# Kernel tuning notes

Hardware: AMD Instinct MI355X
Metric: run time of the kernel (lower is better)

The kernel has to match this reference:

```python
import jax, jax.numpy as jnp
import numpy as np

WIN = 9
EPS = 1e-05


def _box_sum(x, win=WIN):
    # Separable 3D box-filter sum: mathematically identical to conv3d with a
    pad = win // 2
    for axis in range(3):  # spatial axes D, H, W
        kshape = [1, 1, 1]
        kshape[axis] = win
        filt = jnp.ones((1, 1, *kshape), dtype=x.dtype)  # OIDHW
        padding = [(pad, pad) if i == axis else (0, 0) for i in range(3)]
        x = jax.lax.conv_general_dilated(
            x, filt, window_strides=(1, 1, 1), padding=padding,
            dimension_numbers=('NCDHW', 'OIDHW', 'NCDHW'))
    return x


def setup_inputs() -> dict:
    key = jax.random.key(0)
    k1, k2 = jax.random.split(key)
    shape = (2, 1, 160, 192, 224)
    y_true = jax.random.uniform(k1, shape, dtype=jnp.float32)
    y_pred = jax.random.uniform(k2, shape, dtype=jnp.float32)
    return {"y_true": y_true, "y_pred": y_pred}


def reference(y_true, y_pred):
    ii, ji = y_true, y_pred
    win_size = jnp.asarray(float(WIN ** 3), dtype=ii.dtype)

    i_sum = _box_sum(ii)
    j_sum = _box_sum(ji)
    i2_sum = _box_sum(ii * ii)
    j2_sum = _box_sum(ji * ji)
    ij_sum = _box_sum(ii * ji)

    ui = i_sum / win_size
    uj = j_sum / win_size
    cross = ij_sum - uj * i_sum - ui * j_sum + ui * uj * win_size
    i_var = jnp.maximum(i2_sum - 2 * ui * i_sum + ui * ui * win_size, EPS)
    j_var = jnp.maximum(j2_sum - 2 * uj * j_sum + uj * uj * win_size, EPS)
    return -jnp.mean(cross * cross / (i_var * j_var))
```

## Files before the change

kernel.cpp:

```cpp
#include <hip/hip_runtime.h>

namespace {

constexpr int BD = 2;
constexpr int DD = 160, HH = 192, WW = 224;
constexpr float INV_WIN = 1.0f / 729.0f;
constexpr float EPSV = 1e-5f;

constexpr int TH = 16, TW = 16;
constexpr int DC = 16;
constexpr int NREAL = DC + 8;
constexpr int NSS = NREAL / 2;
constexpr int NCH = DD / DC;
constexpr int GX = WW / TW;
constexpr int GY = HH / TH;
constexpr int GZ = BD * NCH;
constexpr int NBLK = GX * GY * GZ;
constexpr double NTOT = (double)BD * DD * HH * WW;

constexpr int SR_FS = 452;
constexpr int SR_PL = 2280;
constexpr int SC_FS = 324;
constexpr int SC_PL = 1620;

}

__global__ __launch_bounds__(256)
void ncc_fused(const float* __restrict__ x, const float* __restrict__ y,
               float* __restrict__ bsum) {
  const int tid = threadIdx.x;
  const int w0 = blockIdx.x * TW;
  const int h0 = blockIdx.y * TH;
  const int zb = blockIdx.z;
  const int b  = zb / NCH;
  const int d0 = (zb - b * NCH) * DC;

  __shared__ __align__(16) float srowF[2 * SR_PL];
  __shared__ __align__(16) float scolF[2 * SC_PL];
  __shared__ float swsum[4];

  const bool s2a = tid < 192;
  const int p2  = tid / 96;
  const int t96 = tid - 96 * p2;
  const int r2  = t96 >> 2;
  const int seg = tid & 3;
  const int gh  = h0 - 4 + r2;
  const int gw0 = w0 - 4 + seg * 4;
  const bool hok = (unsigned)gh < (unsigned)HH;
  const bool fastw = (gw0 >= 0) && (gw0 + 11 < WW);
  const unsigned plane = (unsigned)HH * WW;

  auto prefetch = [&](int s, float4* vx, float4* vy) {
    const int din = d0 - 4 + s;
    const float4 z = make_float4(0.f, 0.f, 0.f, 0.f);
    vx[0] = vx[1] = vx[2] = z;
    vy[0] = vy[1] = vy[2] = z;
    if (s2a && hok && (s < NREAL) && (din >= 0) && (din < DD)) {
      const unsigned rb = ((unsigned)b * DD + (unsigned)din) * plane + (unsigned)gh * WW;
      if (fastw) {
        const float4* px = (const float4*)(x + rb + gw0);
        const float4* py = (const float4*)(y + rb + gw0);
        vx[0] = px[0]; vx[1] = px[1]; vx[2] = px[2];
        vy[0] = py[0]; vy[1] = py[1]; vy[2] = py[2];
      } else {
        float* fx = (float*)vx;
        float* fy = (float*)vy;
#pragma unroll
        for (int e = 0; e < 12; ++e) {
          const int gw = gw0 + e;
          if ((unsigned)gw < (unsigned)WW) {
            fx[e] = x[rb + gw];
            fy[e] = y[rb + gw];
          }
        }
      }
    }
  };

  const int ow = tid & 15;
  const int oh = tid >> 4;

  float rg0[9], rg1[9], rg2[9], rg3[9], rg4[9];
#pragma unroll
  for (int k = 0; k < 9; ++k) { rg0[k]=0.f; rg1[k]=0.f; rg2[k]=0.f; rg3[k]=0.f; rg4[k]=0.f; }
  float a0=0.f, a1=0.f, a2=0.f, a3=0.f, a4=0.f;
  float lsum = 0.0f;

  float4 px4[3], py4[3];
  prefetch(p2, px4, py4);

#pragma unroll
  for (int ss = 0; ss < NSS; ++ss) {
    const int sA = 2 * ss;
    const int sB = sA + 1;
    const int slA = sA % 9;
    const int slB = sB % 9;

    float4 nx4[3], ny4[3];
    prefetch(2 * (ss + 1) + p2, nx4, ny4);

    if (s2a) {
      float xv[12], yv[12];
#pragma unroll
      for (int k = 0; k < 3; ++k) {
        *(float4*)&xv[4 * k] = px4[k];
        *(float4*)&yv[4 * k] = py4[k];
      }
      float s0=0.f, s1=0.f, s2=0.f, s3=0.f, s4=0.f;
#pragma unroll
      for (int k = 0; k < 9; ++k) {
        s0 += xv[k]; s1 += yv[k];
        s2 = fmaf(xv[k], xv[k], s2);
        s3 = fmaf(yv[k], yv[k], s3);
        s4 = fmaf(xv[k], yv[k], s4);
      }
      float* wb = &srowF[p2 * SR_PL + (seg * 4) * 28 + r2];
      wb[0 * SR_FS] = s0; wb[1 * SR_FS] = s1; wb[2 * SR_FS] = s2;
      wb[3 * SR_FS] = s3; wb[4 * SR_FS] = s4;
#pragma unroll
      for (int t = 1; t < 4; ++t) {
        const float xn = xv[8 + t], xo = xv[t - 1];
        const float yn = yv[8 + t], yo = yv[t - 1];
        s0 += xn - xo;
        s1 += yn - yo;
        s2 += fmaf(xn, xn, -(xo * xo));
        s3 += fmaf(yn, yn, -(yo * yo));
        s4 += fmaf(xn, yn, -(xo * yo));
        float* wt = wb + t * 28;
        wt[0 * SR_FS] = s0; wt[1 * SR_FS] = s1; wt[2 * SR_FS] = s2;
        wt[3 * SR_FS] = s3; wt[4 * SR_FS] = s4;
      }
    }
    __syncthreads();

    if (tid < 160) {
      const int p3  = tid / 80;
      const int r3  = tid - 80 * p3;
      const int f3  = r3 >> 4;
      const int wl3 = r3 & 15;
      const float* rp = &srowF[p3 * SR_PL + f3 * SR_FS + wl3 * 28];
      float rv[24];
#pragma unroll
      for (int t = 0; t < 6; ++t) *(float4*)&rv[4 * t] = *(const float4*)&rp[4 * t];
      float acc = rv[0];
#pragma unroll
      for (int t = 1; t < 9; ++t) acc += rv[t];
      float ov[16];
      ov[0] = acc;
#pragma unroll
      for (int o = 1; o < 16; ++o) { acc += rv[o + 8] - rv[o - 1]; ov[o] = acc; }
      float* cp = &scolF[p3 * SC_PL + f3 * SC_FS + wl3 * 20];
#pragma unroll
      for (int t = 0; t < 4; ++t)
        *(float4*)&cp[4 * t] = make_float4(ov[4*t], ov[4*t+1], ov[4*t+2], ov[4*t+3]);
    }
    __syncthreads();

    const float* cA = &scolF[ow * 20 + oh];
    const float* cB = cA + SC_PL;
    const float gA0 = cA[0*SC_FS], gA1 = cA[1*SC_FS], gA2 = cA[2*SC_FS],
                gA3 = cA[3*SC_FS], gA4 = cA[4*SC_FS];
    const float gB0 = cB[0*SC_FS], gB1 = cB[1*SC_FS], gB2 = cB[2*SC_FS],
                gB3 = cB[3*SC_FS], gB4 = cB[4*SC_FS];

    a0 += gA0 - rg0[slA]; rg0[slA] = gA0;
    a1 += gA1 - rg1[slA]; rg1[slA] = gA1;
    a2 += gA2 - rg2[slA]; rg2[slA] = gA2;
    a3 += gA3 - rg3[slA]; rg3[slA] = gA3;
    a4 += gA4 - rg4[slA]; rg4[slA] = gA4;
    if (sA >= 8) {
      const float cross = fmaf(-a0 * INV_WIN, a1, a4);
      const float iv = fmaxf(fmaf(-a0 * INV_WIN, a0, a2), EPSV);
      const float jv = fmaxf(fmaf(-a1 * INV_WIN, a1, a3), EPSV);
      lsum += (cross * cross) / (iv * jv);
    }
    a0 += gB0 - rg0[slB]; rg0[slB] = gB0;
    a1 += gB1 - rg1[slB]; rg1[slB] = gB1;
    a2 += gB2 - rg2[slB]; rg2[slB] = gB2;
    a3 += gB3 - rg3[slB]; rg3[slB] = gB3;
    a4 += gB4 - rg4[slB]; rg4[slB] = gB4;
    if (sB >= 8) {
      const float cross = fmaf(-a0 * INV_WIN, a1, a4);
      const float iv = fmaxf(fmaf(-a0 * INV_WIN, a0, a2), EPSV);
      const float jv = fmaxf(fmaf(-a1 * INV_WIN, a1, a3), EPSV);
      lsum += (cross * cross) / (iv * jv);
    }

#pragma unroll
    for (int k = 0; k < 3; ++k) { px4[k] = nx4[k]; py4[k] = ny4[k]; }
  }

#pragma unroll
  for (int off = 32; off > 0; off >>= 1) lsum += __shfl_down(lsum, off);
  if ((tid & 63) == 0) swsum[tid >> 6] = lsum;
  __syncthreads();
  if (tid == 0) {
    const int bid = ((int)blockIdx.z * GY + (int)blockIdx.y) * GX + (int)blockIdx.x;
    bsum[bid] = swsum[0] + swsum[1] + swsum[2] + swsum[3];
  }
}

__global__ __launch_bounds__(256)
void ncc_finalize(const float* __restrict__ bsum, float* __restrict__ out) {
  double s = 0.0;
  for (int i = threadIdx.x; i < NBLK; i += 256) s += (double)bsum[i];
#pragma unroll
  for (int off = 32; off > 0; off >>= 1) s += __shfl_down(s, off);
  __shared__ double sh[4];
  if ((threadIdx.x & 63) == 0) sh[threadIdx.x >> 6] = s;
  __syncthreads();
  if (threadIdx.x == 0)
    out[0] = (float)(-(sh[0] + sh[1] + sh[2] + sh[3]) / NTOT);
}

extern "C" void kernel_launch(void* const* d_in, const int* in_sizes, int n_in,
                              void* d_out, int out_size, void* d_ws, size_t ws_size,
                              hipStream_t stream) {
  const float* x = (const float*)d_in[0];
  const float* y = (const float*)d_in[1];
  float* bsum = (float*)d_ws;
  float* out  = (float*)d_out;

  dim3 grid(GX, GY, GZ);
  ncc_fused<<<grid, dim3(256), 0, stream>>>(x, y, bsum);
  ncc_finalize<<<1, dim3(256), 0, stream>>>(bsum, out);
}
```

Measured before the change: 211.1 us.

## Software-pipeline row, column and depth stages with one barrier per slice

The old loop handled two depth slices per iteration with two barriers, and all threads waited between the row-sum, column-sum and depth-accumulate stages. The new loop processes one slice per step and staggers the three stages across slices. Warps 0-1 do row sums for slice s, warps 2-3 do column sums for slice s-1, and all threads accumulate depth for slice s-2, with double-buffered shared memory and a single barrier per step. This lets the stages run concurrently on different warps, at the cost of 26 steps instead of 12 and fewer threads doing row sums per step.

```diff
diff --git a/kernel.cpp b/kernel.cpp
--- a/kernel.cpp
+++ b/kernel.cpp
@@ -10,7 +10,7 @@
 constexpr int TH = 16, TW = 16;
 constexpr int DC = 16;
 constexpr int NREAL = DC + 8;
-constexpr int NSS = NREAL / 2;
+constexpr int NSTEP = NREAL + 2;
 constexpr int NCH = DD / DC;
 constexpr int GX = WW / TW;
 constexpr int GY = HH / TH;
@@ -19,9 +19,9 @@
 constexpr double NTOT = (double)BD * DD * HH * WW;
 
 constexpr int SR_FS = 452;
-constexpr int SR_PL = 2280;
+constexpr int SR_BUF = 2280;
 constexpr int SC_FS = 324;
-constexpr int SC_PL = 1620;
+constexpr int SC_BUF = 1620;
 
 }
 
@@ -35,14 +35,12 @@
   const int b  = zb / NCH;
   const int d0 = (zb - b * NCH) * DC;
 
-  __shared__ __align__(16) float srowF[2 * SR_PL];
-  __shared__ __align__(16) float scolF[2 * SC_PL];
+  __shared__ __align__(16) float srowF[2][SR_BUF];
+  __shared__ __align__(16) float scolF[2][SC_BUF];
   __shared__ float swsum[4];
 
-  const bool s2a = tid < 192;
-  const int p2  = tid / 96;
-  const int t96 = tid - 96 * p2;
-  const int r2  = t96 >> 2;
+  const bool s2a = tid < 96;
+  const int r2  = tid >> 2;
   const int seg = tid & 3;
   const int gh  = h0 - 4 + r2;
   const int gw0 = w0 - 4 + seg * 4;
@@ -77,6 +75,11 @@
     }
   };
 
+  const bool s3a = (tid >= 128) && (tid < 208);
+  const int t3  = tid - 128;
+  const int f3  = t3 >> 4;
+  const int wl3 = t3 & 15;
+
   const int ow = tid & 15;
   const int oh = tid >> 4;
 
@@ -87,19 +90,33 @@
   float lsum = 0.0f;
 
   float4 px4[3], py4[3];
-  prefetch(p2, px4, py4);
-
-#pragma unroll
-  for (int ss = 0; ss < NSS; ++ss) {
-    const int sA = 2 * ss;
-    const int sB = sA + 1;
-    const int slA = sA % 9;
-    const int slB = sB % 9;
-
+  prefetch(0, px4, py4);
+
+#pragma unroll
+  for (int s = 0; s < NSTEP; ++s) {
     float4 nx4[3], ny4[3];
-    prefetch(2 * (ss + 1) + p2, nx4, ny4);
-
-    if (s2a) {
+    prefetch(s + 1, nx4, ny4);
+
+    if (s >= 2) {
+      const int ps = s - 2;
+      const int sl = ps % 9;
+      const float* cp = &scolF[ps & 1][ow * 20 + oh];
+      const float g0 = cp[0*SC_FS], g1 = cp[1*SC_FS], g2 = cp[2*SC_FS],
+                  g3 = cp[3*SC_FS], g4 = cp[4*SC_FS];
+      a0 += g0 - rg0[sl]; rg0[sl] = g0;
+      a1 += g1 - rg1[sl]; rg1[sl] = g1;
+      a2 += g2 - rg2[sl]; rg2[sl] = g2;
+      a3 += g3 - rg3[sl]; rg3[sl] = g3;
+      a4 += g4 - rg4[sl]; rg4[sl] = g4;
+      if (ps >= 8) {
+        const float cross = fmaf(-a0 * INV_WIN, a1, a4);
+        const float iv = fmaxf(fmaf(-a0 * INV_WIN, a0, a2), EPSV);
+        const float jv = fmaxf(fmaf(-a1 * INV_WIN, a1, a3), EPSV);
+        lsum += (cross * cross) / (iv * jv);
+      }
+    }
+
+    if (s < NREAL && s2a) {
       float xv[12], yv[12];
 #pragma unroll
       for (int k = 0; k < 3; ++k) {
@@ -114,7 +131,7 @@
         s3 = fmaf(yv[k], yv[k], s3);
         s4 = fmaf(xv[k], yv[k], s4);
       }
-      float* wb = &srowF[p2 * SR_PL + (seg * 4) * 28 + r2];
+      float* wb = &srowF[s & 1][(seg * 4) * 28 + r2];
       wb[0 * SR_FS] = s0; wb[1 * SR_FS] = s1; wb[2 * SR_FS] = s2;
       wb[3 * SR_FS] = s3; wb[4 * SR_FS] = s4;
 #pragma unroll
@@ -131,14 +148,9 @@
         wt[3 * SR_FS] = s3; wt[4 * SR_FS] = s4;
       }
     }
-    __syncthreads();
-
-    if (tid < 160) {
-      const int p3  = tid / 80;
-      const int r3  = tid - 80 * p3;
-      const int f3  = r3 >> 4;
-      const int wl3 = r3 & 15;
-      const float* rp = &srowF[p3 * SR_PL + f3 * SR_FS + wl3 * 28];
+
+    if (s >= 1 && s <= NREAL && s3a) {
+      const float* rp = &srowF[(s - 1) & 1][f3 * SR_FS + wl3 * 28];
       float rv[24];
 #pragma unroll
       for (int t = 0; t < 6; ++t) *(float4*)&rv[4 * t] = *(const float4*)&rp[4 * t];
@@ -149,43 +161,13 @@
       ov[0] = acc;
 #pragma unroll
       for (int o = 1; o < 16; ++o) { acc += rv[o + 8] - rv[o - 1]; ov[o] = acc; }
-      float* cp = &scolF[p3 * SC_PL + f3 * SC_FS + wl3 * 20];
+      float* cp = &scolF[(s - 1) & 1][f3 * SC_FS + wl3 * 20];
 #pragma unroll
       for (int t = 0; t < 4; ++t)
         *(float4*)&cp[4 * t] = make_float4(ov[4*t], ov[4*t+1], ov[4*t+2], ov[4*t+3]);
     }
+
     __syncthreads();
-
-    const float* cA = &scolF[ow * 20 + oh];
-    const float* cB = cA + SC_PL;
-    const float gA0 = cA[0*SC_FS], gA1 = cA[1*SC_FS], gA2 = cA[2*SC_FS],
-                gA3 = cA[3*SC_FS], gA4 = cA[4*SC_FS];
-    const float gB0 = cB[0*SC_FS], gB1 = cB[1*SC_FS], gB2 = cB[2*SC_FS],
-                gB3 = cB[3*SC_FS], gB4 = cB[4*SC_FS];
-
-    a0 += gA0 - rg0[slA]; rg0[slA] = gA0;
-    a1 += gA1 - rg1[slA]; rg1[slA] = gA1;
-    a2 += gA2 - rg2[slA]; rg2[slA] = gA2;
-    a3 += gA3 - rg3[slA]; rg3[slA] = gA3;
-    a4 += gA4 - rg4[slA]; rg4[slA] = gA4;
-    if (sA >= 8) {
-      const float cross = fmaf(-a0 * INV_WIN, a1, a4);
-      const float iv = fmaxf(fmaf(-a0 * INV_WIN, a0, a2), EPSV);
-      const float jv = fmaxf(fmaf(-a1 * INV_WIN, a1, a3), EPSV);
-      lsum += (cross * cross) / (iv * jv);
-    }
-    a0 += gB0 - rg0[slB]; rg0[slB] = gB0;
-    a1 += gB1 - rg1[slB]; rg1[slB] = gB1;
-    a2 += gB2 - rg2[slB]; rg2[slB] = gB2;
-    a3 += gB3 - rg3[slB]; rg3[slB] = gB3;
-    a4 += gB4 - rg4[slB]; rg4[slB] = gB4;
-    if (sB >= 8) {
-      const float cross = fmaf(-a0 * INV_WIN, a1, a4);
-      const float iv = fmaxf(fmaf(-a0 * INV_WIN, a0, a2), EPSV);
-      const float jv = fmaxf(fmaf(-a1 * INV_WIN, a1, a3), EPSV);
-      lsum += (cross * cross) / (iv * jv);
-    }
-
 #pragma unroll
     for (int k = 0; k < 3; ++k) { px4[k] = nx4[k]; py4[k] = ny4[k]; }
   }
```

New measurement: 263.1 us. 24.6% more time.
